# Kernel tuning notes

Measured on AMD Instinct MI355X. Metric: run time of the kernel, lower is better.

Reference implementation:

```python
import jax, jax.numpy as jnp
import numpy as np


def _rot_mat(thetas, scales):
    # thetas, scales: [bs, g] -> [bs, g, 9, 9] bilinear-interpolation matrices
    bs, g = thetas.shape
    t = thetas.reshape(-1)
    s = scales.reshape(-1)
    x = jnp.cos(t) * s
    y = jnp.sin(t) * s
    yp = -y
    z = jnp.zeros_like(x)
    o = jnp.ones_like(x)
    a = x - y; b = x * y; c = x + y; d = a * c; e = a + c
    ap = x - yp; bp = x * yp; cp = x + yp; dp = ap * cp; ep = ap + cp

    def M(rows):
        # rows: 9 lists of 9 [N]-arrays -> [9, 9, N]
        return jnp.stack([jnp.stack(r, axis=0) for r in rows], axis=0)

    ctr = [z, z, z, z, o, z, z, z, z]

    pb1 = M([
        [a, 1 - a, z, z, z, z, z, z, z],
        [z, 1 - y, y, z, z, z, z, z, z],
        [z, z, a, z, z, 1 - a, z, z, z],
        [y, z, z, 1 - y, z, z, z, z, z],
        ctr,
        [z, z, z, z, z, 1 - y, z, z, y],
        [z, z, z, 1 - a, z, z, a, z, z],
        [z, z, z, z, z, z, y, 1 - y, z],
        [z, z, z, z, z, z, z, 1 - a, a]])
    pb2 = M([
        [a, 1 - a, z, z, z, z, z, z, z],
        [z, x - b, b, z, 1 - c + b, y - b, z, z, z],
        [z, z, a, z, z, 1 - a, z, z, z],
        [b, y - b, z, x - b, 1 - c + b, z, z, z, z],
        ctr,
        [z, z, z, z, 1 - c + b, x - b, z, y - b, b],
        [z, z, z, 1 - a, z, z, a, z, z],
        [z, z, z, y - b, 1 - c + b, z, b, x - b, z],
        [z, z, z, z, z, z, z, 1 - a, a]])
    ps1 = M([
        [d, a - d, z, c - d, 1 - e + d, z, z, z, z],
        [z, x - b, b, z, 1 - c + b, y - b, z, z, z],
        [z, c - d, d, z, 1 - e + d, a - d, z, z, z],
        [b, y - b, z, x - b, 1 - c + b, z, z, z, z],
        ctr,
        [z, z, z, z, 1 - c + b, x - b, z, y - b, b],
        [z, z, z, a - d, 1 - e + d, z, d, c - d, z],
        [z, z, z, y - b, 1 - c + b, z, b, x - b, z],
        [z, z, z, z, 1 - e + d, c - d, z, a - d, d]])
    ps2 = pb2  # identical in the source
    nb1 = M([
        [cp, z, z, 1 - cp, z, z, z, z, z],
        [yp, 1 - yp, z, z, z, z, z, z, z],
        [z, 1 - cp, cp, z, z, z, z, z, z],
        [z, z, z, 1 - yp, z, z, yp, z, z],
        ctr,
        [z, z, yp, z, z, 1 - yp, z, z, z],
        [z, z, z, z, z, z, cp, 1 - cp, z],
        [z, z, z, z, z, z, z, 1 - yp, yp],
        [z, z, z, z, z, 1 - cp, z, z, cp]])
    nb2 = M([
        [cp, z, z, 1 - cp, z, z, z, z, z],
        [bp, x - bp, z, yp - bp, 1 - cp + bp, z, z, z, z],
        [z, 1 - cp, cp, z, z, z, z, z, z],
        [z, z, z, x - bp, 1 - cp + bp, z, bp, yp - bp, z],
        ctr,
        [z, yp - bp, bp, z, 1 - cp + bp, x - bp, z, z, z],
        [z, z, z, z, z, z, cp, 1 - cp, z],
        [z, z, z, z, 1 - cp + bp, yp - bp, z, x - bp, bp],
        [z, z, z, z, z, 1 - cp, z, z, cp]])
    ns1 = M([
        [dp, cp - dp, z, ap - dp, 1 - ep + dp, z, z, z, z],
        [bp, x - bp, z, yp - bp, 1 - cp + bp, z, z, z, z],
        [z, ap - dp, dp, z, 1 - ep + dp, cp - dp, z, z, z],
        [z, yp - bp, bp, z, 1 - cp + bp, x - bp, z, z, z],
        ctr,
        [z, z, z, x - bp, 1 - cp + bp, z, bp, yp - bp, z],
        [z, z, z, cp - dp, 1 - ep + dp, z, dp, ap - dp, z],
        [z, z, z, z, 1 - cp + bp, yp - bp, z, x - bp, bp],
        [z, z, z, z, 1 - ep + dp, ap - dp, z, cp - dp, dp]])
    ns2 = nb2  # mirrors the positive branch where small_2 == big_2

    m_pos = (t >= 0.0)[None, None, :]
    m_big = (s >= 1.0)[None, None, :]
    m_1 = (jnp.abs(t) <= jnp.pi / 4)[None, None, :]
    pos = jnp.where(m_big, jnp.where(m_1, pb1, pb2), jnp.where(m_1, ps1, ps2))
    neg = jnp.where(m_big, jnp.where(m_1, nb1, nb2), jnp.where(m_1, ns1, ns2))
    rot = jnp.where(m_pos, pos, neg)  # [9, 9, bs*g]
    return jnp.transpose(rot, (2, 0, 1)).reshape(bs, g, 9, 9)


def _forward(x, thetas, scales, lambdas, weight):
    # x: [B, Cin, H, W]; weight: [n, Cout, Cin, 3, 3]; thetas/scales/lambdas: [B, n]
    B, Cin, H, W = x.shape
    n, Cout = weight.shape[0], weight.shape[1]
    rot = _rot_mat(thetas, scales) * lambdas[:, :, None, None]  # [B, n, 9, 9]
    w9 = weight.reshape(n, Cout, Cin, 9)
    # per-sample transformed kernel: sum over kernel_number n and source taps j
    w = jnp.einsum('bnij,nocj->bioc', rot, w9)  # [B, 9, Cout, Cin]
    w = jnp.transpose(w, (0, 2, 3, 1)).reshape(B * Cout, Cin, 3, 3)
    xg = x.reshape(1, B * Cin, H, W)
    out = jax.lax.conv_general_dilated(
        xg, w, window_strides=(1, 1), padding=((1, 1), (1, 1)),
        dimension_numbers=('NCHW', 'OIHW', 'NCHW'), feature_group_count=B)
    return out.reshape(B, Cout, H, W)


def setup_inputs() -> dict:
    key = jax.random.key(0)
    ks = jax.random.split(key, 5)
    B, Cin, Cout, H, W, n = 16, 256, 256, 64, 64, 4
    x = jax.random.normal(ks[0], (B, Cin, H, W), dtype=jnp.float32)
    thetas = jax.random.uniform(ks[1], (B, n), minval=-1.2, maxval=1.2, dtype=jnp.float32)
    scales = jax.random.uniform(ks[2], (B, n), minval=0.5, maxval=1.5, dtype=jnp.float32)
    lambdas = jax.nn.softmax(jax.random.normal(ks[3], (B, n), dtype=jnp.float32), axis=-1)
    weight = jax.random.normal(ks[4], (n, Cout, Cin, 3, 3), dtype=jnp.float32) * 0.05
    return {"x": x, "thetas": thetas, "scales": scales, "lambdas": lambdas, "weight": weight}


def reference(x, thetas, scales, lambdas, weight):
    return _forward(x, thetas, scales, lambdas, weight)
```

## Files before the change

kernel.cpp:

```cpp
#include <hip/hip_runtime.h>
#include <cstdint>
#include <cstddef>

typedef unsigned short ushort_t;
typedef __attribute__((ext_vector_type(4))) float f32x4;
typedef __attribute__((ext_vector_type(8))) short s16x8;

#define PI_4F 0.78539816339744830962f

__device__ inline ushort_t f2bf(float f) {
  unsigned int u = __float_as_uint(f);
  u = u + 0x7fffu + ((u >> 16) & 1u);
  return (ushort_t)(u >> 16);
}

__device__ void rot_compute(float t, float s, float* M) {
  float xv = cosf(t) * s, yv = sinf(t) * s;
  bool pos = (t >= 0.0f), big = (s >= 1.0f), m1 = (fabsf(t) <= PI_4F);
#pragma unroll
  for (int i = 0; i < 81; ++i) M[i] = 0.0f;
  M[36 + 4] = 1.0f;
  if (pos) {
    float a = xv - yv, bb = xv * yv, c = xv + yv;
    if (m1 && big) {
      M[0] = a; M[1] = 1 - a;
      M[9 + 1] = 1 - yv; M[9 + 2] = yv;
      M[18 + 2] = a; M[18 + 5] = 1 - a;
      M[27 + 0] = yv; M[27 + 3] = 1 - yv;
      M[45 + 5] = 1 - yv; M[45 + 8] = yv;
      M[54 + 3] = 1 - a; M[54 + 6] = a;
      M[63 + 6] = yv; M[63 + 7] = 1 - yv;
      M[72 + 7] = 1 - a; M[72 + 8] = a;
    } else if (m1) {
      float d = a * c, e = a + c;
      M[0] = d; M[1] = a - d; M[3] = c - d; M[4] = 1 - e + d;
      M[9 + 1] = xv - bb; M[9 + 2] = bb; M[9 + 4] = 1 - c + bb; M[9 + 5] = yv - bb;
      M[18 + 1] = c - d; M[18 + 2] = d; M[18 + 4] = 1 - e + d; M[18 + 5] = a - d;
      M[27 + 0] = bb; M[27 + 1] = yv - bb; M[27 + 3] = xv - bb; M[27 + 4] = 1 - c + bb;
      M[45 + 4] = 1 - c + bb; M[45 + 5] = xv - bb; M[45 + 7] = yv - bb; M[45 + 8] = bb;
      M[54 + 3] = a - d; M[54 + 4] = 1 - e + d; M[54 + 6] = d; M[54 + 7] = c - d;
      M[63 + 3] = yv - bb; M[63 + 4] = 1 - c + bb; M[63 + 6] = bb; M[63 + 7] = xv - bb;
      M[72 + 4] = 1 - e + d; M[72 + 5] = c - d; M[72 + 7] = a - d; M[72 + 8] = d;
    } else {
      M[0] = a; M[1] = 1 - a;
      M[9 + 1] = xv - bb; M[9 + 2] = bb; M[9 + 4] = 1 - c + bb; M[9 + 5] = yv - bb;
      M[18 + 2] = a; M[18 + 5] = 1 - a;
      M[27 + 0] = bb; M[27 + 1] = yv - bb; M[27 + 3] = xv - bb; M[27 + 4] = 1 - c + bb;
      M[45 + 4] = 1 - c + bb; M[45 + 5] = xv - bb; M[45 + 7] = yv - bb; M[45 + 8] = bb;
      M[54 + 3] = 1 - a; M[54 + 6] = a;
      M[63 + 3] = yv - bb; M[63 + 4] = 1 - c + bb; M[63 + 6] = bb; M[63 + 7] = xv - bb;
      M[72 + 7] = 1 - a; M[72 + 8] = a;
    }
  } else {
    float yp = -yv;
    float ap = xv - yp, bp = xv * yp, cp = xv + yp;
    if (m1 && big) {
      M[0] = cp; M[3] = 1 - cp;
      M[9 + 0] = yp; M[9 + 1] = 1 - yp;
      M[18 + 1] = 1 - cp; M[18 + 2] = cp;
      M[27 + 3] = 1 - yp; M[27 + 6] = yp;
      M[45 + 2] = yp; M[45 + 5] = 1 - yp;
      M[54 + 6] = cp; M[54 + 7] = 1 - cp;
      M[63 + 7] = 1 - yp; M[63 + 8] = yp;
      M[72 + 5] = 1 - cp; M[72 + 8] = cp;
    } else if (m1) {
      float dp = ap * cp, ep = ap + cp;
      M[0] = dp; M[1] = cp - dp; M[3] = ap - dp; M[4] = 1 - ep + dp;
      M[9 + 0] = bp; M[9 + 1] = xv - bp; M[9 + 3] = yp - bp; M[9 + 4] = 1 - cp + bp;
      M[18 + 1] = ap - dp; M[18 + 2] = dp; M[18 + 4] = 1 - ep + dp; M[18 + 5] = cp - dp;
      M[27 + 1] = yp - bp; M[27 + 2] = bp; M[27 + 4] = 1 - cp + bp; M[27 + 5] = xv - bp;
      M[45 + 3] = xv - bp; M[45 + 4] = 1 - cp + bp; M[45 + 6] = bp; M[45 + 7] = yp - bp;
      M[54 + 3] = cp - dp; M[54 + 4] = 1 - ep + dp; M[54 + 6] = dp; M[54 + 7] = ap - dp;
      M[63 + 4] = 1 - cp + bp; M[63 + 5] = yp - bp; M[63 + 7] = xv - bp; M[63 + 8] = bp;
      M[72 + 4] = 1 - ep + dp; M[72 + 5] = ap - dp; M[72 + 7] = cp - dp; M[72 + 8] = dp;
    } else {
      M[0] = cp; M[3] = 1 - cp;
      M[9 + 0] = bp; M[9 + 1] = xv - bp; M[9 + 3] = yp - bp; M[9 + 4] = 1 - cp + bp;
      M[18 + 1] = 1 - cp; M[18 + 2] = cp;
      M[27 + 3] = xv - bp; M[27 + 4] = 1 - cp + bp; M[27 + 6] = bp; M[27 + 7] = yp - bp;
      M[45 + 1] = yp - bp; M[45 + 2] = bp; M[45 + 4] = 1 - cp + bp; M[45 + 5] = xv - bp;
      M[54 + 6] = cp; M[54 + 7] = 1 - cp;
      M[63 + 4] = 1 - cp + bp; M[63 + 5] = yp - bp; M[63 + 7] = xv - bp; M[63 + 8] = bp;
      M[72 + 5] = 1 - cp; M[72 + 8] = cp;
    }
  }
}

__global__ __launch_bounds__(256) void prep_kernel(
    const float* __restrict__ x, const float* __restrict__ weight,
    const float* __restrict__ thetas, const float* __restrict__ scales,
    const float* __restrict__ lambdas, ushort_t* __restrict__ xpad,
    ushort_t* __restrict__ wtout) {
  __shared__ __align__(16) char smem[32 * 81 * 4];
  const int bi = blockIdx.x;
  const int t = threadIdx.x;

  if (bi < 256) {
    float* rotl = (float*)smem;
    const int o2 = bi & 127, bq = bi >> 7;
    const int half = t >> 7, tloc = t & 127;
    const int o = o2 * 2 + half;
    const int c = tloc * 2;
    float wv0[4][9], wv1[4][9];
#pragma unroll
    for (int n = 0; n < 4; ++n) {
      const float* wp = weight + (((size_t)(n * 256 + o)) * 256 + c) * 9;
#pragma unroll
      for (int j = 0; j < 9; ++j) { wv0[n][j] = wp[j]; wv1[n][j] = wp[9 + j]; }
    }
    if (t < 32) {
      int gid = bq * 32 + t;
      float M[81];
      rot_compute(thetas[gid], scales[gid], M);
      float lam = lambdas[gid];
#pragma unroll
      for (int i = 0; i < 81; ++i) rotl[t * 81 + i] = M[i] * lam;
    }
    __syncthreads();
#pragma unroll
    for (int bl = 0; bl < 8; ++bl) {
      const int b = bq * 8 + bl;
#pragma unroll
      for (int i = 0; i < 9; ++i) {
        float a0 = 0.0f, a1 = 0.0f;
#pragma unroll
        for (int n = 0; n < 4; ++n) {
          const float* r = &rotl[(bl * 4 + n) * 81 + i * 9];
#pragma unroll
          for (int j = 0; j < 9; ++j) {
            a0 = fmaf(r[j], wv0[n][j], a0);
            a1 = fmaf(r[j], wv1[n][j], a1);
          }
        }
        unsigned int word = (unsigned int)f2bf(a0) | ((unsigned int)f2bf(a1) << 16);
        *(unsigned int*)&wtout[((size_t)((b * 9 + i) * 256 + o)) * 256 + c] = word;
      }
    }
  } else {
    ushort_t (*tile)[68] = (ushort_t(*)[68])smem;
    const int bi2 = bi - 256;
    const int b = bi2 >> 8, ct = (bi2 >> 6) & 3, st = bi2 & 63;
    const int c0 = ct * 64;
    const float* xb = x + ((size_t)(b * 256 + c0)) * 4096 + st * 64;
#pragma unroll
    for (int k = 0; k < 4; ++k) {
      int idx = t + 256 * k;
      int c_l = idx >> 4, w4 = (idx & 15) * 4;
      float4 v = *(const float4*)&xb[(size_t)c_l * 4096 + w4];
      tile[w4 + 0][c_l] = f2bf(v.x);
      tile[w4 + 1][c_l] = f2bf(v.y);
      tile[w4 + 2][c_l] = f2bf(v.z);
      tile[w4 + 3][c_l] = f2bf(v.w);
    }
    __syncthreads();
    const int c4 = (t & 15) * 4, wl = t >> 4;
    const size_t rowbase = (size_t)(b * 4356 + (st + 1) * 66) * 256 + c0;
#pragma unroll
    for (int k = 0; k < 4; ++k) {
      int w = wl + 16 * k;
      uint2 v = *(const uint2*)&tile[w][c4];
      *(uint2*)&xpad[rowbase + (size_t)(w + 1) * 256 + c4] = v;
    }
    if (t < 32) {
      int w = (t & 16) ? 65 : 0;
      int cc = (t & 15) * 4;
      *(uint2*)&xpad[rowbase + (size_t)w * 256 + cc] = make_uint2(0u, 0u);
    }
    if (st == 0 || st == 63) {
      const int h = (st == 0) ? 0 : 65;
      const size_t hb = (size_t)(b * 4356 + h * 66) * 256 + c0;
      for (int idx = t; idx < 66 * 16; idx += 256) {
        int w = idx >> 4, cc = (idx & 15) * 4;
        *(uint2*)&xpad[hb + (size_t)w * 256 + cc] = make_uint2(0u, 0u);
      }
    }
  }
}

__device__ inline void gload16(const ushort_t* g, ushort_t* l) {
  __builtin_amdgcn_global_load_lds(
      (const __attribute__((address_space(1))) unsigned int*)g,
      (__attribute__((address_space(3))) unsigned int*)l, 16, 0, 0);
}

#define WAITB(N)                                                      \
  asm volatile("s_waitcnt vmcnt(" #N ") lgkmcnt(0)\n\ts_barrier" ::: "memory")

__global__ __launch_bounds__(256, 2) void conv_kernel(
    const ushort_t* __restrict__ xpad, const ushort_t* __restrict__ wt,
    float* __restrict__ out) {
  __shared__ __align__(16) ushort_t As0[8192], As1[8192], As2[8192];
  __shared__ __align__(16) ushort_t Bs0[4096], Bs1[4096], Bs2[4096];

  const int id = blockIdx.x;
  const int xcd = id & 7;
  const int jj = id >> 3;
  const int b = xcd * 2 + (jj >> 5);
  const int ntile = jj & 31;

  const int t = threadIdx.x;
  const int wave = t >> 6, lane = t & 63;
  const int wm = wave & 1, wn = wave >> 1;
  const int lr = lane & 15, lq = lane >> 4;
  const int h0 = ntile * 2;

  const ushort_t* wt_b = wt + (size_t)b * 589824;
  const ushort_t* xp_b = xpad + (size_t)b * 1115136;

  const int lrow = t >> 2;
  const int cg8 = (((t & 3) ^ ((t >> 3) & 3)) * 8);
  const int rsw = (lr >> 1) & 3;
  const int aoff = (wm * 128 + lr) * 32 + ((lq ^ rsw) * 8);
  const int boff = (wn * 64 + lr) * 32 + ((lq ^ rsw) * 8);

  f32x4 acc[8][4];
#pragma unroll
  for (int i = 0; i < 8; ++i)
#pragma unroll
    for (int j2 = 0; j2 < 4; ++j2) acc[i][j2] = (f32x4)(0.0f);

  auto stage = [&](int ks, ushort_t* Ad, ushort_t* Bd) {
    const int tap = ks >> 3;
    const int c0k = (ks & 7) << 5;
    const int kh = tap / 3, kw = tap - kh * 3;
    const ushort_t* ga = wt_b + ((size_t)(tap * 256 + lrow)) * 256 + c0k + cg8;
    gload16(ga, Ad + wave * 512);
    gload16(ga + 64 * 256, Ad + 2048 + wave * 512);
    gload16(ga + 128 * 256, Ad + 4096 + wave * 512);
    gload16(ga + 192 * 256, Ad + 6144 + wave * 512);
    const int sp = (h0 + kh) * 66 + kw + lrow;
    gload16(xp_b + (size_t)sp * 256 + c0k + cg8, Bd + wave * 512);
    gload16(xp_b + (size_t)(sp + 66) * 256 + c0k + cg8, Bd + 2048 + wave * 512);
  };

  auto compute = [&](const ushort_t* Ab, const ushort_t* Bb) {
    s16x8 bfr[4];
#pragma unroll
    for (int ni = 0; ni < 4; ++ni)
      bfr[ni] = *(const s16x8*)(Bb + boff + ni * 512);
#pragma unroll
    for (int mi = 0; mi < 8; ++mi) {
      s16x8 af = *(const s16x8*)(Ab + aoff + mi * 512);
#pragma unroll
      for (int ni = 0; ni < 4; ++ni)
        acc[mi][ni] = __builtin_amdgcn_mfma_f32_16x16x32_bf16(af, bfr[ni], acc[mi][ni], 0, 0, 0);
    }
  };

  stage(0, As0, Bs0);
  stage(1, As1, Bs1);

#pragma unroll 1
  for (int kk = 0; kk < 23; ++kk) {
    const int ks = kk * 3;
    WAITB(6);
    stage(ks + 2, As2, Bs2);
    compute(As0, Bs0);
    WAITB(6);
    stage(ks + 3, As0, Bs0);
    compute(As1, Bs1);
    WAITB(6);
    stage(ks + 4, As1, Bs1);
    compute(As2, Bs2);
  }
  WAITB(6);
  stage(71, As2, Bs2);
  compute(As0, Bs0);
  WAITB(6);
  compute(As1, Bs1);
  WAITB(0);
  compute(As2, Bs2);

  float* ob = out + ((size_t)(b * 256 + wm * 128)) * 4096 + ntile * 128 + wn * 64 + lr;
#pragma unroll
  for (int mi = 0; mi < 8; ++mi)
#pragma unroll
    for (int r = 0; r < 4; ++r) {
      float* orow = ob + (size_t)(mi * 16 + lq * 4 + r) * 4096;
#pragma unroll
      for (int ni = 0; ni < 4; ++ni) orow[ni * 16] = acc[mi][ni][r];
    }
}

extern "C" void kernel_launch(void* const* d_in, const int* in_sizes, int n_in,
                              void* d_out, int out_size, void* d_ws, size_t ws_size,
                              hipStream_t stream) {
  const float* x = (const float*)d_in[0];
  const float* thetas = (const float*)d_in[1];
  const float* scales = (const float*)d_in[2];
  const float* lambdas = (const float*)d_in[3];
  const float* weight = (const float*)d_in[4];
  float* out = (float*)d_out;

  ushort_t* wt_ws = (ushort_t*)d_ws;
  ushort_t* xpad_ws = (ushort_t*)((char*)d_ws + 18874368);

  prep_kernel<<<4352, 256, 0, stream>>>(x, weight, thetas, scales, lambdas,
                                        xpad_ws, wt_ws);
  conv_kernel<<<512, 256, 0, stream>>>(xpad_ws, wt_ws, out);
}
```

Measured before the change: 214.5 us.

## Split each k-step into two MFMA halves interleaved with staged loads and priority

Each pipeline step is split into two halves. A-tile global-to-LDS loads are issued before the first half of MFMAs and B-tile loads before the second half. Extra barriers keep the waves in lockstep, and s_setprio raises wave priority around the MFMA blocks, in the style of ping-pong scheduling. The aim is to spread memory issue across compute and overlap LDS reads with MFMA work. The cost is more barriers per step and more fragment registers held live.

Result: no change. 215.1 us (+0.3%).

```diff
diff --git a/kernel.cpp b/kernel.cpp
--- a/kernel.cpp
+++ b/kernel.cpp
@@ -185,6 +185,7 @@
 
 #define WAITB(N)                                                      \
   asm volatile("s_waitcnt vmcnt(" #N ") lgkmcnt(0)\n\ts_barrier" ::: "memory")
+#define BAR() asm volatile("s_barrier" ::: "memory")
 
 __global__ __launch_bounds__(256, 2) void conv_kernel(
     const ushort_t* __restrict__ xpad, const ushort_t* __restrict__ wt,
@@ -219,57 +220,73 @@
 #pragma unroll
     for (int j2 = 0; j2 < 4; ++j2) acc[i][j2] = (f32x4)(0.0f);
 
-  auto stage = [&](int ks, ushort_t* Ad, ushort_t* Bd) {
+  auto stage_A = [&](int ks, ushort_t* Ad) {
     const int tap = ks >> 3;
     const int c0k = (ks & 7) << 5;
-    const int kh = tap / 3, kw = tap - kh * 3;
     const ushort_t* ga = wt_b + ((size_t)(tap * 256 + lrow)) * 256 + c0k + cg8;
     gload16(ga, Ad + wave * 512);
     gload16(ga + 64 * 256, Ad + 2048 + wave * 512);
     gload16(ga + 128 * 256, Ad + 4096 + wave * 512);
     gload16(ga + 192 * 256, Ad + 6144 + wave * 512);
+  };
+  auto stage_B = [&](int ks, ushort_t* Bd) {
+    const int tap = ks >> 3;
+    const int c0k = (ks & 7) << 5;
+    const int kh = tap / 3, kw = tap - kh * 3;
     const int sp = (h0 + kh) * 66 + kw + lrow;
     gload16(xp_b + (size_t)sp * 256 + c0k + cg8, Bd + wave * 512);
     gload16(xp_b + (size_t)(sp + 66) * 256 + c0k + cg8, Bd + 2048 + wave * 512);
   };
 
-  auto compute = [&](const ushort_t* Ab, const ushort_t* Bb) {
-    s16x8 bfr[4];
-#pragma unroll
-    for (int ni = 0; ni < 4; ++ni)
-      bfr[ni] = *(const s16x8*)(Bb + boff + ni * 512);
-#pragma unroll
-    for (int mi = 0; mi < 8; ++mi) {
-      s16x8 af = *(const s16x8*)(Ab + aoff + mi * 512);
+  auto step = [&](const ushort_t* cA, const ushort_t* cB, ushort_t* nA,
+                  ushort_t* nB, int ks2, bool do_stage) {
+    s16x8 bfr[4], afA[4], afB[4];
+    if (do_stage) stage_A(ks2, nA);
+#pragma unroll
+    for (int ni = 0; ni < 4; ++ni) bfr[ni] = *(const s16x8*)(cB + boff + ni * 512);
+#pragma unroll
+    for (int mi = 0; mi < 4; ++mi) afA[mi] = *(const s16x8*)(cA + aoff + mi * 512);
+    BAR();
+    __builtin_amdgcn_s_setprio(1);
+#pragma unroll
+    for (int mi = 0; mi < 4; ++mi)
 #pragma unroll
       for (int ni = 0; ni < 4; ++ni)
-        acc[mi][ni] = __builtin_amdgcn_mfma_f32_16x16x32_bf16(af, bfr[ni], acc[mi][ni], 0, 0, 0);
-    }
+        acc[mi][ni] = __builtin_amdgcn_mfma_f32_16x16x32_bf16(afA[mi], bfr[ni], acc[mi][ni], 0, 0, 0);
+    __builtin_amdgcn_s_setprio(0);
+    BAR();
+    if (do_stage) stage_B(ks2, nB);
+#pragma unroll
+    for (int mi = 0; mi < 4; ++mi) afB[mi] = *(const s16x8*)(cA + aoff + (mi + 4) * 512);
+    BAR();
+    __builtin_amdgcn_s_setprio(1);
+#pragma unroll
+    for (int mi = 0; mi < 4; ++mi)
+#pragma unroll
+      for (int ni = 0; ni < 4; ++ni)
+        acc[mi + 4][ni] = __builtin_amdgcn_mfma_f32_16x16x32_bf16(afB[mi], bfr[ni], acc[mi + 4][ni], 0, 0, 0);
+    __builtin_amdgcn_s_setprio(0);
   };
 
-  stage(0, As0, Bs0);
-  stage(1, As1, Bs1);
+  stage_A(0, As0); stage_B(0, Bs0);
+  stage_A(1, As1); stage_B(1, Bs1);
 
 #pragma unroll 1
   for (int kk = 0; kk < 23; ++kk) {
     const int ks = kk * 3;
     WAITB(6);
-    stage(ks + 2, As2, Bs2);
-    compute(As0, Bs0);
+    step(As0, Bs0, As2, Bs2, ks + 2, true);
     WAITB(6);
-    stage(ks + 3, As0, Bs0);
-    compute(As1, Bs1);
+    step(As1, Bs1, As0, Bs0, ks + 3, true);
     WAITB(6);
-    stage(ks + 4, As1, Bs1);
-    compute(As2, Bs2);
+    step(As2, Bs2, As1, Bs1, ks + 4, true);
   }
   WAITB(6);
-  stage(71, As2, Bs2);
-  compute(As0, Bs0);
+  step(As0, Bs0, As2, Bs2, 71, true);
   WAITB(6);
-  compute(As1, Bs1);
+  step(As1, Bs1, nullptr, nullptr, 0, false);
   WAITB(0);
-  compute(As2, Bs2);
+  step(As2, Bs2, nullptr, nullptr, 0, false);
 
   float* ob = out + ((size_t)(b * 256 + wm * 128)) * 4096 + ntile * 128 + wn * 64 + lr;
 #pragma unroll
```

## Load weight operand directly into registers, keep only activations in LDS

Applied to the files above, without the earlier changes.

The weight (A) tiles no longer go through LDS. Each wave now loads its own A fragments from global memory straight into a double-buffered register array, one k-step ahead. Only the activation (B) tiles stay in the triple-buffered LDS pipeline, and the loop is restructured into a uniform 72-step schedule with a fixed vmcnt(2) wait. This removes the LDS writes and reads for A and cuts shared memory use, at the cost of duplicate global/L2 reads across waves that share the same A rows, more VGPR pressure, and only one step of latency hiding for the A loads.

Measured after the change: 284.0 us. 32.4% more time.

```diff
diff --git a/kernel.cpp b/kernel.cpp
--- a/kernel.cpp
+++ b/kernel.cpp
@@ -183,13 +183,12 @@
       (__attribute__((address_space(3))) unsigned int*)l, 16, 0, 0);
 }
 
-#define WAITB(N)                                                      \
-  asm volatile("s_waitcnt vmcnt(" #N ") lgkmcnt(0)\n\ts_barrier" ::: "memory")
+#define WAITB2()                                                      \
+  asm volatile("s_waitcnt vmcnt(2) lgkmcnt(0)\n\ts_barrier" ::: "memory")
 
 __global__ __launch_bounds__(256, 2) void conv_kernel(
     const ushort_t* __restrict__ xpad, const ushort_t* __restrict__ wt,
     float* __restrict__ out) {
-  __shared__ __align__(16) ushort_t As0[8192], As1[8192], As2[8192];
   __shared__ __align__(16) ushort_t Bs0[4096], Bs1[4096], Bs2[4096];
 
   const int id = blockIdx.x;
@@ -210,8 +209,8 @@
   const int lrow = t >> 2;
   const int cg8 = (((t & 3) ^ ((t >> 3) & 3)) * 8);
   const int rsw = (lr >> 1) & 3;
-  const int aoff = (wm * 128 + lr) * 32 + ((lq ^ rsw) * 8);
   const int boff = (wn * 64 + lr) * 32 + ((lq ^ rsw) * 8);
+  const ushort_t* wa_base = wt_b + ((size_t)(wm * 128 + lr)) * 256 + lq * 8;
 
   f32x4 acc[8][4];
 #pragma unroll
@@ -219,57 +218,58 @@
 #pragma unroll
     for (int j2 = 0; j2 < 4; ++j2) acc[i][j2] = (f32x4)(0.0f);
 
-  auto stage = [&](int ks, ushort_t* Ad, ushort_t* Bd) {
+  s16x8 afA[8], afB[8];
+
+  auto loadA = [&](int ks, s16x8* af) {
+    const int tap = ks >> 3;
+    const int c0k = (ks & 7) << 5;
+    const ushort_t* ga = wa_base + (size_t)tap * 65536 + c0k;
+#pragma unroll
+    for (int mi = 0; mi < 8; ++mi)
+      af[mi] = *(const s16x8*)(ga + mi * 4096);
+  };
+
+  auto stage_B = [&](int ks, ushort_t* Bd) {
     const int tap = ks >> 3;
     const int c0k = (ks & 7) << 5;
     const int kh = tap / 3, kw = tap - kh * 3;
-    const ushort_t* ga = wt_b + ((size_t)(tap * 256 + lrow)) * 256 + c0k + cg8;
-    gload16(ga, Ad + wave * 512);
-    gload16(ga + 64 * 256, Ad + 2048 + wave * 512);
-    gload16(ga + 128 * 256, Ad + 4096 + wave * 512);
-    gload16(ga + 192 * 256, Ad + 6144 + wave * 512);
     const int sp = (h0 + kh) * 66 + kw + lrow;
     gload16(xp_b + (size_t)sp * 256 + c0k + cg8, Bd + wave * 512);
     gload16(xp_b + (size_t)(sp + 66) * 256 + c0k + cg8, Bd + 2048 + wave * 512);
   };
 
-  auto compute = [&](const ushort_t* Ab, const ushort_t* Bb) {
+  auto step = [&](int ks, const ushort_t* Bcur, ushort_t* Bstage,
+                  const s16x8* afCur, s16x8* afNxt) {
+    WAITB2();
+    const int a1 = (ks + 1 > 71) ? 71 : ks + 1;
+    const int b2 = (ks + 2 > 71) ? 71 : ks + 2;
+    loadA(a1, afNxt);
+    stage_B(b2, Bstage);
     s16x8 bfr[4];
 #pragma unroll
     for (int ni = 0; ni < 4; ++ni)
-      bfr[ni] = *(const s16x8*)(Bb + boff + ni * 512);
-#pragma unroll
-    for (int mi = 0; mi < 8; ++mi) {
-      s16x8 af = *(const s16x8*)(Ab + aoff + mi * 512);
+      bfr[ni] = *(const s16x8*)(Bcur + boff + ni * 512);
+#pragma unroll
+    for (int mi = 0; mi < 8; ++mi)
 #pragma unroll
       for (int ni = 0; ni < 4; ++ni)
-        acc[mi][ni] = __builtin_amdgcn_mfma_f32_16x16x32_bf16(af, bfr[ni], acc[mi][ni], 0, 0, 0);
-    }
+        acc[mi][ni] = __builtin_amdgcn_mfma_f32_16x16x32_bf16(afCur[mi], bfr[ni], acc[mi][ni], 0, 0, 0);
   };
 
-  stage(0, As0, Bs0);
-  stage(1, As1, Bs1);
+  stage_B(0, Bs0);
+  loadA(0, afA);
+  stage_B(1, Bs1);
 
 #pragma unroll 1
-  for (int kk = 0; kk < 23; ++kk) {
-    const int ks = kk * 3;
-    WAITB(6);
-    stage(ks + 2, As2, Bs2);
-    compute(As0, Bs0);
-    WAITB(6);
-    stage(ks + 3, As0, Bs0);
-    compute(As1, Bs1);
-    WAITB(6);
-    stage(ks + 4, As1, Bs1);
-    compute(As2, Bs2);
+  for (int kk = 0; kk < 12; ++kk) {
+    const int ks = kk * 6;
+    step(ks + 0, Bs0, Bs2, afA, afB);
+    step(ks + 1, Bs1, Bs0, afB, afA);
+    step(ks + 2, Bs2, Bs1, afA, afB);
+    step(ks + 3, Bs0, Bs2, afB, afA);
+    step(ks + 4, Bs1, Bs0, afA, afB);
+    step(ks + 5, Bs2, Bs1, afB, afA);
   }
-  WAITB(6);
-  stage(71, As2, Bs2);
-  compute(As0, Bs0);
-  WAITB(6);
-  compute(As1, Bs1);
-  WAITB(0);
-  compute(As2, Bs2);
 
   float* ob = out + ((size_t)(b * 256 + wm * 128)) * 4096 + ntile * 128 + wn * 64 + lr;
 #pragma unroll
```
